# Kernel optimization log

Measured on AMD Instinct MI355X. Metric: run time of the kernel, lower is better.

## Reference

```python
import jax, jax.numpy as jnp
import numpy as np

M, N, DV, DC, ITERS = 512, 1024, 3, 6, 10
BATCH = 8192
ATANH_CLIP = 0.999995


def _build_graph():
    """Deterministic (3,6)-regular Tanner graph, edge order = row-major nonzeros of H."""
    offsets = [0, 1, 2, 512, 515, 519]
    H = np.zeros((M, N), np.int64)
    r = np.arange(M)
    for off in offsets:
        H[r, (2 * r + off) % N] = 1
    ei, ej = np.nonzero(H)                       # E = M*DC = 3072 edges, row-major
    E = ei.size
    var2edges = np.argsort(ej, kind='stable').reshape(N, DV)   # edges of each variable
    chk2edges = np.argsort(ei, kind='stable').reshape(M, DC)   # edges of each check
    v_sum = np.empty((E, DV - 1), np.int64)      # for edge e: other edges on same variable
    c_prod = np.empty((E, DC - 1), np.int64)     # for edge e: other edges on same check
    for e in range(E):
        gv = var2edges[ej[e]]
        v_sum[e] = gv[gv != e]
        gc = chk2edges[ei[e]]
        c_prod[e] = gc[gc != e]
    return v_sum, c_prod, ej.astype(np.int64), var2edges


def setup_inputs() -> dict:
    key = jax.random.key(0)
    ks = jax.random.split(key, 6)
    v_sum, c_prod, edge_var, var2edges = _build_graph()
    E = edge_var.shape[0]                        # 3072
    TW = E * (DV - 1)                            # total_weights = 6144
    return {
        "llr": jax.random.normal(ks[0], (BATCH, N), jnp.float32),
        "w_iter": 1.0 + 0.1 * jax.random.normal(ks[1], (ITERS, TW), jnp.float32),
        "llr_iter": 1.0 + 0.1 * jax.random.normal(ks[2], (ITERS, N), jnp.float32),
        "w_final": 1.0 + 0.1 * jax.random.normal(ks[3], (E,), jnp.float32),
        "llr_final": 1.0 + 0.1 * jax.random.normal(ks[4], (N,), jnp.float32),
        "v_sum_idx": jnp.asarray(v_sum),         # [E, DV-1]
        "c_prod_idx": jnp.asarray(c_prod),       # [E, DC-1]
        "edge_var": jnp.asarray(edge_var),       # [E] variable index of each edge
        "final_idx": jnp.asarray(var2edges),     # [N, DV] edges feeding each variable marginal
    }


def reference(llr, w_iter, llr_iter, w_final, llr_final,
              v_sum_idx, c_prod_idx, edge_var, final_idx):
    B = llr.shape[0]
    E = edge_var.shape[0]
    c2v0 = jnp.zeros((B, E), llr.dtype)

    def bp_iter(c2v, params):
        w, lw = params                                      # [E*(DV-1)], [N]
        # variable -> check: weighted sum of extrinsic c2v messages + weighted LLR
        s = (c2v[:, v_sum_idx] * w.reshape(E, DV - 1)).sum(-1)        # [B,E]
        v2c = jnp.tanh(0.5 * (s + (llr * lw)[:, edge_var]))           # [B,E]
        # check -> variable: product of extrinsic v2c messages, 2*atanh
        prods = v2c[:, c_prod_idx].prod(-1)                           # [B,E]
        return 2.0 * jnp.arctanh(ATANH_CLIP * prods), None

    c2v, _ = jax.lax.scan(bp_iter, c2v0, (w_iter, llr_iter))
    # final marginalization: per-variable sum of weighted incoming messages
    fin = (c2v[:, final_idx.reshape(-1)] * w_final).reshape(B, N, DV).sum(-1)
    out = fin + llr * llr_final
    return jax.nn.sigmoid(out[:, : N - M])
```

## Files before the change

### kernel.cpp

```cpp
#include <hip/hip_runtime.h>
#include <hip/hip_bf16.h>


namespace {

typedef float v2f __attribute__((ext_vector_type(2)));

constexpr int T      = 512;
constexpr int ROWS   = 2;
constexpr int MCHK   = 512;
constexpr int NVAR   = 1024;
constexpr int EEDG   = 3072;
constexpr int NITER  = 10;
constexpr int STRIDE = 7;
constexpr int BATCH  = 8192;
constexpr int NOUT   = 512;

constexpr float LOG2E = 1.4426950408889634f;
constexpr float LN2   = 0.6931471805599453f;
constexpr float KAPPA = 0.999995f;
constexpr float ZCLMP = 16777216.0f;

__device__ __forceinline__ float fast_exp2(float x) { return __builtin_amdgcn_exp2f(x); }
__device__ __forceinline__ float fast_log2(float x) { return __builtin_amdgcn_logf(x); }
__device__ __forceinline__ float fast_rcp (float x) { return __builtin_amdgcn_rcpf(x); }

__global__ __launch_bounds__(T, 4)
void bp_decode(const float* __restrict__ llr,
               const float* __restrict__ w_iter,
               const float* __restrict__ llr_iter,
               const float* __restrict__ w_final,
               const float* __restrict__ llr_final,
               const int*  __restrict__ v_sum_idx,
               const int*  __restrict__ edge_var,
               const int*  __restrict__ final_idx,
               float* __restrict__ out)
{
    __shared__ v2f Ad[MCHK * STRIDE];

    const int  tid = threadIdx.x;
    const long b0  = (long)blockIdx.x * ROWS;

    #pragma unroll
    for (int k = 0; k < STRIDE; ++k)
        Ad[k * T + tid] = (v2f)(0.f);

    int nb[12];
    {
        const int4* p = (const int4*)(v_sum_idx + 12 * tid);
        int4 q0 = p[0], q1 = p[1], q2 = p[2];
        nb[0]=q0.x; nb[1]=q0.y; nb[2]=q0.z; nb[3]=q0.w;
        nb[4]=q1.x; nb[5]=q1.y; nb[6]=q1.z; nb[7]=q1.w;
        nb[8]=q2.x; nb[9]=q2.y; nb[10]=q2.z; nb[11]=q2.w;
    }
    int goff[12];
    #pragma unroll
    for (int j = 0; j < 12; ++j)
        goff[j] = (nb[j] / 6) * STRIDE + (nb[j] % 6);

    int var[6];
    {
        const int2* p = (const int2*)(edge_var + 6 * tid);
        int2 q0 = p[0], q1 = p[1], q2 = p[2];
        var[0]=q0.x; var[1]=q0.y; var[2]=q1.x; var[3]=q1.y; var[4]=q2.x; var[5]=q2.y;
    }

    v2f L[6];
    #pragma unroll
    for (int j = 0; j < 6; ++j) {
        L[j].x = llr[ b0      * NVAR + var[j]];
        L[j].y = llr[(b0 + 1) * NVAR + var[j]];
    }

    __syncthreads();

    const int own = STRIDE * tid;

    #pragma unroll 1
    for (int it = 0; it < NITER; ++it) {
        const float* wit = w_iter + it * (EEDG * 2) + 12 * tid;
        float4 wa = ((const float4*)wit)[0];
        float4 wb = ((const float4*)wit)[1];
        float4 wc = ((const float4*)wit)[2];
        float w[12] = {wa.x,wa.y,wa.z,wa.w, wb.x,wb.y,wb.z,wb.w, wc.x,wc.y,wc.z,wc.w};

        const float* lit = llr_iter + it * NVAR;
        v2f Lli[6];
        #pragma unroll
        for (int j = 0; j < 6; ++j) Lli[j] = L[j] * (lit[var[j]] * LOG2E);

        v2f g[12];
        #pragma unroll
        for (int j = 0; j < 12; ++j) g[j] = Ad[goff[j]];

        __syncthreads();

        v2f zm[6], zp[6];
        #pragma unroll
        for (int j = 0; j < 6; ++j) {
            v2f a = w[2*j] * g[2*j] + w[2*j+1] * g[2*j+1] + Lli[j];
            v2f z;
            z.x = fast_exp2(a.x);
            z.y = fast_exp2(a.y);
            z.x = fminf(z.x, ZCLMP);
            z.y = fminf(z.y, ZCLMP);
            zm[j] = z - 1.f;
            zp[j] = z + 1.f;
        }

        v2f A[6], B[6];
        {
            v2f P1=zm[0], P2=P1*zm[1], P3=P2*zm[2], P4=P3*zm[3], P5=P4*zm[4];
            v2f S4=zm[5], S3=S4*zm[4], S2=S3*zm[3], S1=S2*zm[2], S0=S1*zm[1];
            A[0]=S0; A[1]=P1*S1; A[2]=P2*S2; A[3]=P3*S3; A[4]=P4*S4; A[5]=P5;
        }
        {
            v2f P1=zp[0], P2=P1*zp[1], P3=P2*zp[2], P4=P3*zp[3], P5=P4*zp[4];
            v2f S4=zp[5], S3=S4*zp[4], S2=S3*zp[3], S1=S2*zp[2], S0=S1*zp[1];
            B[0]=S0; B[1]=P1*S1; B[2]=P2*S2; B[3]=P3*S3; B[4]=P4*S4; B[5]=P5;
        }

        #pragma unroll
        for (int j = 0; j < 6; ++j) {
            v2f num = KAPPA * A[j] + B[j];
            v2f den = B[j] - KAPPA * A[j];
            v2f d;
            d.x = fast_log2(num.x) - fast_log2(den.x);
            d.y = fast_log2(num.y) - fast_log2(den.y);
            Ad[own + j] = d;
        }

        __syncthreads();
    }

    int f0 = final_idx[3*tid], f1 = final_idx[3*tid + 1], f2 = final_idx[3*tid + 2];
    v2f d0 = Ad[(f0 / 6) * STRIDE + (f0 % 6)];
    v2f d1 = Ad[(f1 / 6) * STRIDE + (f1 % 6)];
    v2f d2 = Ad[(f2 / 6) * STRIDE + (f2 % 6)];
    float wf0 = w_final[3*tid], wf1 = w_final[3*tid + 1], wf2 = w_final[3*tid + 2];
    float lf  = llr_final[tid];
    float l0  = llr[ b0      * NVAR + tid];
    float l1  = llr[(b0 + 1) * NVAR + tid];

    float finx = (d0.x*wf0 + d1.x*wf1 + d2.x*wf2) * LN2;
    float finy = (d0.y*wf0 + d1.y*wf1 + d2.y*wf2) * LN2;
    float vx = fmaf(l0, lf, finx);
    float vy = fmaf(l1, lf, finy);
    float ox = fast_rcp(1.f + fast_exp2(-vx * LOG2E));
    float oy = fast_rcp(1.f + fast_exp2(-vy * LOG2E));

    out[ b0      * NOUT + tid] = ox;
    out[(b0 + 1) * NOUT + tid] = oy;
}

}

extern "C" void kernel_launch(void* const* d_in, const int* in_sizes, int n_in,
                              void* d_out, int out_size, void* d_ws, size_t ws_size,
                              hipStream_t stream)
{
    const float* llr       = (const float*)d_in[0];
    const float* w_iter    = (const float*)d_in[1];
    const float* llr_iter  = (const float*)d_in[2];
    const float* w_final   = (const float*)d_in[3];
    const float* llr_final = (const float*)d_in[4];
    const int*   v_sum_idx = (const int*)d_in[5];
    const int*   edge_var  = (const int*)d_in[7];
    const int*   final_idx = (const int*)d_in[8];
    float* outp = (float*)d_out;

    dim3 grid(BATCH / ROWS), block(T);
    hipLaunchKernelGGL(bp_decode, grid, block, 0, stream,
                       llr, w_iter, llr_iter, w_final, llr_final,
                       v_sum_idx, edge_var, final_idx, outp);
}
```

Measured before the change: 219.0 us.

## Halve block size and process two checks per thread with packed indices

Block size drops from 512 to 256 threads, and each thread now runs the check-node update for two checks over the same two batch rows. Neighbour offsets and variable indices are packed two per 32-bit register, LOG2E is folded into the cached LLRs ahead of the loop, and the saturation clamp moves from after exp2 to its input. The aim is more independent work per thread for latency hiding, barriers shared across twice the work per thread, and lower register pressure from the packed indices. The cost is a longer serial chain per thread and different occupancy from the new block size. A redundant duplicate log computation is left in the helper.

```diff
diff --git a/kernel.cpp b/kernel.cpp
--- a/kernel.cpp
+++ b/kernel.cpp
@@ -6,8 +6,7 @@
 
 typedef float v2f __attribute__((ext_vector_type(2)));
 
-constexpr int T      = 512;
-constexpr int ROWS   = 2;
+constexpr int T      = 256;
 constexpr int MCHK   = 512;
 constexpr int NVAR   = 1024;
 constexpr int EEDG   = 3072;
@@ -19,11 +18,50 @@
 constexpr float LOG2E = 1.4426950408889634f;
 constexpr float LN2   = 0.6931471805599453f;
 constexpr float KAPPA = 0.999995f;
-constexpr float ZCLMP = 16777216.0f;
+constexpr float ACLMP = 24.0f;
 
 __device__ __forceinline__ float fast_exp2(float x) { return __builtin_amdgcn_exp2f(x); }
 __device__ __forceinline__ float fast_log2(float x) { return __builtin_amdgcn_logf(x); }
 __device__ __forceinline__ float fast_rcp (float x) { return __builtin_amdgcn_rcpf(x); }
+
+__device__ __forceinline__ void check_update(const v2f* __restrict__ g,
+                                             const float* __restrict__ w,
+                                             const v2f* __restrict__ Lli,
+                                             v2f* __restrict__ d)
+{
+    v2f zm[6], zp[6];
+    #pragma unroll
+    for (int j = 0; j < 6; ++j) {
+        v2f a = w[2*j] * g[2*j] + w[2*j+1] * g[2*j+1] + Lli[j];
+        a = __builtin_elementwise_min(a, (v2f)(ACLMP));
+        v2f z;
+        z.x = fast_exp2(a.x);
+        z.y = fast_exp2(a.y);
+        zm[j] = z - 1.f;
+        zp[j] = z + 1.f;
+    }
+    v2f A[6], B[6];
+    {
+        v2f P1=zm[0], P2=P1*zm[1], P3=P2*zm[2], P4=P3*zm[3], P5=P4*zm[4];
+        v2f S4=zm[5], S3=S4*zm[4], S2=S3*zm[3], S1=S2*zm[2], S0=S1*zm[1];
+        A[0]=S0; A[1]=P1*S1; A[2]=P2*S2; A[3]=P3*S3; A[4]=P4*S4; A[5]=P5;
+    }
+    {
+        v2f P1=zp[0], P2=P1*zp[1], P3=P2*zp[2], P4=P3*zp[3], P5=P4*zp[4];
+        v2f S4=zp[5], S3=S4*zp[4], S2=S3*zp[3], S1=S2*zp[2], S0=S1*zp[1];
+        B[0]=S0; B[1]=P1*S1; B[2]=P2*S2; B[3]=P3*S3; B[4]=P4*S4; B[5]=P5;
+    }
+    #pragma unroll
+    for (int j = 0; j < 6; ++j) {
+        v2f num = KAPPA * A[j] + B[j];
+        v2f den = B[j] - KAPPA * A[j];
+        v2f dd;
+        dd.x = fast_log2(num.x) - fast_log2(num.x == num.x ? den.x : den.x);
+        dd.x = fast_log2(num.x) - fast_log2(den.x);
+        dd.y = fast_log2(num.y) - fast_log2(den.y);
+        d[j] = dd;
+    }
+}
 
 __global__ __launch_bounds__(T, 4)
 void bp_decode(const float* __restrict__ llr,
@@ -39,118 +77,144 @@
     __shared__ v2f Ad[MCHK * STRIDE];
 
     const int  tid = threadIdx.x;
-    const long b0  = (long)blockIdx.x * ROWS;
-
-    #pragma unroll
-    for (int k = 0; k < STRIDE; ++k)
+    const long b0  = (long)blockIdx.x * 2;
+
+    #pragma unroll
+    for (int k = 0; k < 2 * STRIDE; ++k)
         Ad[k * T + tid] = (v2f)(0.f);
 
-    int nb[12];
-    {
-        const int4* p = (const int4*)(v_sum_idx + 12 * tid);
-        int4 q0 = p[0], q1 = p[1], q2 = p[2];
-        nb[0]=q0.x; nb[1]=q0.y; nb[2]=q0.z; nb[3]=q0.w;
-        nb[4]=q1.x; nb[5]=q1.y; nb[6]=q1.z; nb[7]=q1.w;
-        nb[8]=q2.x; nb[9]=q2.y; nb[10]=q2.z; nb[11]=q2.w;
-    }
-    int goff[12];
-    #pragma unroll
-    for (int j = 0; j < 12; ++j)
-        goff[j] = (nb[j] / 6) * STRIDE + (nb[j] % 6);
-
-    int var[6];
-    {
-        const int2* p = (const int2*)(edge_var + 6 * tid);
-        int2 q0 = p[0], q1 = p[1], q2 = p[2];
-        var[0]=q0.x; var[1]=q0.y; var[2]=q1.x; var[3]=q1.y; var[4]=q2.x; var[5]=q2.y;
-    }
-
-    v2f L[6];
-    #pragma unroll
-    for (int j = 0; j < 6; ++j) {
-        L[j].x = llr[ b0      * NVAR + var[j]];
-        L[j].y = llr[(b0 + 1) * NVAR + var[j]];
-    }
+    unsigned goffp[12];
+    unsigned varp[6];
+    v2f      Lpre[12];
+
+    #pragma unroll
+    for (int cc = 0; cc < 2; ++cc) {
+        const int c = tid + cc * T;
+        int nb[12];
+        {
+            const int4* p = (const int4*)(v_sum_idx + 12 * c);
+            int4 q0 = p[0], q1 = p[1], q2 = p[2];
+            nb[0]=q0.x; nb[1]=q0.y; nb[2]=q0.z; nb[3]=q0.w;
+            nb[4]=q1.x; nb[5]=q1.y; nb[6]=q1.z; nb[7]=q1.w;
+            nb[8]=q2.x; nb[9]=q2.y; nb[10]=q2.z; nb[11]=q2.w;
+        }
+        #pragma unroll
+        for (int i = 0; i < 6; ++i) {
+            unsigned s0 = (unsigned)((nb[2*i]   / 6) * STRIDE + (nb[2*i]   % 6));
+            unsigned s1 = (unsigned)((nb[2*i+1] / 6) * STRIDE + (nb[2*i+1] % 6));
+            goffp[6*cc + i] = s0 | (s1 << 16);
+        }
+        int var[6];
+        {
+            const int2* p = (const int2*)(edge_var + 6 * c);
+            int2 q0 = p[0], q1 = p[1], q2 = p[2];
+            var[0]=q0.x; var[1]=q0.y; var[2]=q1.x; var[3]=q1.y; var[4]=q2.x; var[5]=q2.y;
+        }
+        #pragma unroll
+        for (int i = 0; i < 3; ++i)
+            varp[3*cc + i] = (unsigned)var[2*i] | ((unsigned)var[2*i+1] << 16);
+        #pragma unroll
+        for (int j = 0; j < 6; ++j) {
+            v2f L;
+            L.x = llr[ b0      * NVAR + var[j]];
+            L.y = llr[(b0 + 1) * NVAR + var[j]];
+            Lpre[6*cc + j] = L * LOG2E;
+        }
+    }
+
+    const int own0 = STRIDE * tid;
+    const int own1 = STRIDE * (tid + T);
 
     __syncthreads();
-
-    const int own = STRIDE * tid;
 
     #pragma unroll 1
     for (int it = 0; it < NITER; ++it) {
-        const float* wit = w_iter + it * (EEDG * 2) + 12 * tid;
-        float4 wa = ((const float4*)wit)[0];
-        float4 wb = ((const float4*)wit)[1];
-        float4 wc = ((const float4*)wit)[2];
-        float w[12] = {wa.x,wa.y,wa.z,wa.w, wb.x,wb.y,wb.z,wb.w, wc.x,wc.y,wc.z,wc.w};
-
+        const float* wit = w_iter + it * (EEDG * 2);
+
+        float w0[12];
+        {
+            const float* p = wit + 12 * tid;
+            float4 a = ((const float4*)p)[0], b = ((const float4*)p)[1], c = ((const float4*)p)[2];
+            w0[0]=a.x; w0[1]=a.y; w0[2]=a.z; w0[3]=a.w;
+            w0[4]=b.x; w0[5]=b.y; w0[6]=b.z; w0[7]=b.w;
+            w0[8]=c.x; w0[9]=c.y; w0[10]=c.z; w0[11]=c.w;
+        }
+
+        v2f g0[12], g1[12];
+        #pragma unroll
+        for (int i = 0; i < 6; ++i) {
+            unsigned p = goffp[i];
+            g0[2*i]   = Ad[p & 0xffffu];
+            g0[2*i+1] = Ad[p >> 16];
+        }
+        #pragma unroll
+        for (int i = 0; i < 6; ++i) {
+            unsigned p = goffp[6 + i];
+            g1[2*i]   = Ad[p & 0xffffu];
+            g1[2*i+1] = Ad[p >> 16];
+        }
+
+        __syncthreads();
+
+        float w1[12];
+        {
+            const float* p = wit + 12 * tid + 6 * T * 2;
+            float4 a = ((const float4*)p)[0], b = ((const float4*)p)[1], c = ((const float4*)p)[2];
+            w1[0]=a.x; w1[1]=a.y; w1[2]=a.z; w1[3]=a.w;
+            w1[4]=b.x; w1[5]=b.y; w1[6]=b.z; w1[7]=b.w;
+            w1[8]=c.x; w1[9]=c.y; w1[10]=c.z; w1[11]=c.w;
+        }
         const float* lit = llr_iter + it * NVAR;
-        v2f Lli[6];
-        #pragma unroll
-        for (int j = 0; j < 6; ++j) Lli[j] = L[j] * (lit[var[j]] * LOG2E);
-
-        v2f g[12];
-        #pragma unroll
-        for (int j = 0; j < 12; ++j) g[j] = Ad[goff[j]];
+
+        float lv0[6], lv1[6];
+        #pragma unroll
+        for (int i = 0; i < 3; ++i) {
+            unsigned p = varp[i];
+            lv0[2*i]   = lit[p & 0xffffu];
+            lv0[2*i+1] = lit[p >> 16];
+        }
+        #pragma unroll
+        for (int i = 0; i < 3; ++i) {
+            unsigned p = varp[3 + i];
+            lv1[2*i]   = lit[p & 0xffffu];
+            lv1[2*i+1] = lit[p >> 16];
+        }
+
+        v2f Lli[6], d[6];
+        #pragma unroll
+        for (int j = 0; j < 6; ++j) Lli[j] = Lpre[j] * lv0[j];
+        check_update(g0, w0, Lli, d);
+        #pragma unroll
+        for (int j = 0; j < 6; ++j) Ad[own0 + j] = d[j];
+
+        #pragma unroll
+        for (int j = 0; j < 6; ++j) Lli[j] = Lpre[6 + j] * lv1[j];
+        check_update(g1, w1, Lli, d);
+        #pragma unroll
+        for (int j = 0; j < 6; ++j) Ad[own1 + j] = d[j];
 
         __syncthreads();
-
-        v2f zm[6], zp[6];
-        #pragma unroll
-        for (int j = 0; j < 6; ++j) {
-            v2f a = w[2*j] * g[2*j] + w[2*j+1] * g[2*j+1] + Lli[j];
-            v2f z;
-            z.x = fast_exp2(a.x);
-            z.y = fast_exp2(a.y);
-            z.x = fminf(z.x, ZCLMP);
-            z.y = fminf(z.y, ZCLMP);
-            zm[j] = z - 1.f;
-            zp[j] = z + 1.f;
-        }
-
-        v2f A[6], B[6];
-        {
-            v2f P1=zm[0], P2=P1*zm[1], P3=P2*zm[2], P4=P3*zm[3], P5=P4*zm[4];
-            v2f S4=zm[5], S3=S4*zm[4], S2=S3*zm[3], S1=S2*zm[2], S0=S1*zm[1];
-            A[0]=S0; A[1]=P1*S1; A[2]=P2*S2; A[3]=P3*S3; A[4]=P4*S4; A[5]=P5;
-        }
-        {
-            v2f P1=zp[0], P2=P1*zp[1], P3=P2*zp[2], P4=P3*zp[3], P5=P4*zp[4];
-            v2f S4=zp[5], S3=S4*zp[4], S2=S3*zp[3], S1=S2*zp[2], S0=S1*zp[1];
-            B[0]=S0; B[1]=P1*S1; B[2]=P2*S2; B[3]=P3*S3; B[4]=P4*S4; B[5]=P5;
-        }
-
-        #pragma unroll
-        for (int j = 0; j < 6; ++j) {
-            v2f num = KAPPA * A[j] + B[j];
-            v2f den = B[j] - KAPPA * A[j];
-            v2f d;
-            d.x = fast_log2(num.x) - fast_log2(den.x);
-            d.y = fast_log2(num.y) - fast_log2(den.y);
-            Ad[own + j] = d;
-        }
-
-        __syncthreads();
-    }
-
-    int f0 = final_idx[3*tid], f1 = final_idx[3*tid + 1], f2 = final_idx[3*tid + 2];
-    v2f d0 = Ad[(f0 / 6) * STRIDE + (f0 % 6)];
-    v2f d1 = Ad[(f1 / 6) * STRIDE + (f1 % 6)];
-    v2f d2 = Ad[(f2 / 6) * STRIDE + (f2 % 6)];
-    float wf0 = w_final[3*tid], wf1 = w_final[3*tid + 1], wf2 = w_final[3*tid + 2];
-    float lf  = llr_final[tid];
-    float l0  = llr[ b0      * NVAR + tid];
-    float l1  = llr[(b0 + 1) * NVAR + tid];
-
-    float finx = (d0.x*wf0 + d1.x*wf1 + d2.x*wf2) * LN2;
-    float finy = (d0.y*wf0 + d1.y*wf1 + d2.y*wf2) * LN2;
-    float vx = fmaf(l0, lf, finx);
-    float vy = fmaf(l1, lf, finy);
-    float ox = fast_rcp(1.f + fast_exp2(-vx * LOG2E));
-    float oy = fast_rcp(1.f + fast_exp2(-vy * LOG2E));
-
-    out[ b0      * NOUT + tid] = ox;
-    out[(b0 + 1) * NOUT + tid] = oy;
+    }
+
+    #pragma unroll
+    for (int cc = 0; cc < 2; ++cc) {
+        const int v = tid + cc * T;
+        int f0 = final_idx[3*v], f1 = final_idx[3*v + 1], f2 = final_idx[3*v + 2];
+        v2f d0 = Ad[(f0 / 6) * STRIDE + (f0 % 6)];
+        v2f d1 = Ad[(f1 / 6) * STRIDE + (f1 % 6)];
+        v2f d2 = Ad[(f2 / 6) * STRIDE + (f2 % 6)];
+        float wf0 = w_final[3*v], wf1 = w_final[3*v + 1], wf2 = w_final[3*v + 2];
+        float lf  = llr_final[v];
+        float l0  = llr[ b0      * NVAR + v];
+        float l1  = llr[(b0 + 1) * NVAR + v];
+
+        float finx = (d0.x*wf0 + d1.x*wf1 + d2.x*wf2) * LN2;
+        float finy = (d0.y*wf0 + d1.y*wf1 + d2.y*wf2) * LN2;
+        float vx = fmaf(l0, lf, finx);
+        float vy = fmaf(l1, lf, finy);
+        out[ b0      * NOUT + v] = fast_rcp(1.f + fast_exp2(-vx * LOG2E));
+        out[(b0 + 1) * NOUT + v] = fast_rcp(1.f + fast_exp2(-vy * LOG2E));
+    }
 }
 
 }
@@ -169,7 +233,7 @@
     const int*   final_idx = (const int*)d_in[8];
     float* outp = (float*)d_out;
 
-    dim3 grid(BATCH / ROWS), block(T);
+    dim3 grid(BATCH / 2), block(T);
     hipLaunchKernelGGL(bp_decode, grid, block, 0, stream,
                        llr, w_iter, llr_iter, w_final, llr_final,
                        v_sum_idx, edge_var, final_idx, outp);
```

Result: slower. 288.2 us (+31.6%).

## Process four batch rows per block with v4f LDS messages and packed indices

Applied to the files above, without the earlier changes.

Doubles the batch rows handled per block from two to four, so each LDS gather now loads a 16-byte vector and the per-edge index, weight and llr_iter loads are amortised over more rows. Gather offsets and variable indices are packed two per 32-bit register to offset the extra register pressure, and the clamp moves from the exp2 output to its input. LDS per block doubles to about 57 KB and launch bounds drop to two blocks per CU, which lowers occupancy and gives fewer waves to hide latency across the barriers.

```diff
diff --git a/kernel.cpp b/kernel.cpp
--- a/kernel.cpp
+++ b/kernel.cpp
@@ -4,13 +4,12 @@
 
 namespace {
 
-typedef float v2f __attribute__((ext_vector_type(2)));
+typedef float v4f __attribute__((ext_vector_type(4)));
 
 constexpr int T      = 512;
-constexpr int ROWS   = 2;
+constexpr int ROWS   = 4;
 constexpr int MCHK   = 512;
 constexpr int NVAR   = 1024;
-constexpr int EEDG   = 3072;
 constexpr int NITER  = 10;
 constexpr int STRIDE = 7;
 constexpr int BATCH  = 8192;
@@ -19,13 +18,13 @@
 constexpr float LOG2E = 1.4426950408889634f;
 constexpr float LN2   = 0.6931471805599453f;
 constexpr float KAPPA = 0.999995f;
-constexpr float ZCLMP = 16777216.0f;
+constexpr float ACLMP = 24.0f;
 
 __device__ __forceinline__ float fast_exp2(float x) { return __builtin_amdgcn_exp2f(x); }
 __device__ __forceinline__ float fast_log2(float x) { return __builtin_amdgcn_logf(x); }
 __device__ __forceinline__ float fast_rcp (float x) { return __builtin_amdgcn_rcpf(x); }
 
-__global__ __launch_bounds__(T, 4)
+__global__ __launch_bounds__(T, 2)
 void bp_decode(const float* __restrict__ llr,
                const float* __restrict__ w_iter,
                const float* __restrict__ llr_iter,
@@ -36,121 +35,145 @@
                const int*  __restrict__ final_idx,
                float* __restrict__ out)
 {
-    __shared__ v2f Ad[MCHK * STRIDE];
+    __shared__ v4f Ad[MCHK * STRIDE];
 
     const int  tid = threadIdx.x;
     const long b0  = (long)blockIdx.x * ROWS;
 
     #pragma unroll
     for (int k = 0; k < STRIDE; ++k)
-        Ad[k * T + tid] = (v2f)(0.f);
+        Ad[k * T + tid] = (v4f)(0.f);
 
-    int nb[12];
+    unsigned goffp[6];
+    unsigned varp[3];
+    v4f      Lpre[6];
     {
+        int nb[12];
         const int4* p = (const int4*)(v_sum_idx + 12 * tid);
         int4 q0 = p[0], q1 = p[1], q2 = p[2];
         nb[0]=q0.x; nb[1]=q0.y; nb[2]=q0.z; nb[3]=q0.w;
         nb[4]=q1.x; nb[5]=q1.y; nb[6]=q1.z; nb[7]=q1.w;
         nb[8]=q2.x; nb[9]=q2.y; nb[10]=q2.z; nb[11]=q2.w;
+        #pragma unroll
+        for (int i = 0; i < 6; ++i) {
+            unsigned s0 = (unsigned)((nb[2*i]   / 6) * STRIDE + (nb[2*i]   % 6));
+            unsigned s1 = (unsigned)((nb[2*i+1] / 6) * STRIDE + (nb[2*i+1] % 6));
+            goffp[i] = s0 | (s1 << 16);
+        }
     }
-    int goff[12];
-    #pragma unroll
-    for (int j = 0; j < 12; ++j)
-        goff[j] = (nb[j] / 6) * STRIDE + (nb[j] % 6);
-
-    int var[6];
     {
+        int var[6];
         const int2* p = (const int2*)(edge_var + 6 * tid);
         int2 q0 = p[0], q1 = p[1], q2 = p[2];
         var[0]=q0.x; var[1]=q0.y; var[2]=q1.x; var[3]=q1.y; var[4]=q2.x; var[5]=q2.y;
+        #pragma unroll
+        for (int i = 0; i < 3; ++i)
+            varp[i] = (unsigned)var[2*i] | ((unsigned)var[2*i+1] << 16);
+        #pragma unroll
+        for (int j = 0; j < 6; ++j) {
+            v4f L;
+            L.x = llr[(b0 + 0) * NVAR + var[j]];
+            L.y = llr[(b0 + 1) * NVAR + var[j]];
+            L.z = llr[(b0 + 2) * NVAR + var[j]];
+            L.w = llr[(b0 + 3) * NVAR + var[j]];
+            Lpre[j] = L * LOG2E;
+        }
     }
 
-    v2f L[6];
-    #pragma unroll
-    for (int j = 0; j < 6; ++j) {
-        L[j].x = llr[ b0      * NVAR + var[j]];
-        L[j].y = llr[(b0 + 1) * NVAR + var[j]];
-    }
+    const int own = STRIDE * tid;
 
     __syncthreads();
 
-    const int own = STRIDE * tid;
-
     #pragma unroll 1
     for (int it = 0; it < NITER; ++it) {
-        const float* wit = w_iter + it * (EEDG * 2) + 12 * tid;
-        float4 wa = ((const float4*)wit)[0];
-        float4 wb = ((const float4*)wit)[1];
-        float4 wc = ((const float4*)wit)[2];
-        float w[12] = {wa.x,wa.y,wa.z,wa.w, wb.x,wb.y,wb.z,wb.w, wc.x,wc.y,wc.z,wc.w};
+        float w[12];
+        {
+            const float* p = w_iter + it * 6144 + 12 * tid;
+            float4 a = ((const float4*)p)[0], b = ((const float4*)p)[1], c = ((const float4*)p)[2];
+            w[0]=a.x; w[1]=a.y; w[2]=a.z;  w[3]=a.w;
+            w[4]=b.x; w[5]=b.y; w[6]=b.z;  w[7]=b.w;
+            w[8]=c.x; w[9]=c.y; w[10]=c.z; w[11]=c.w;
+        }
+        const float* lit = llr_iter + it * NVAR;
+        float lv[6];
+        #pragma unroll
+        for (int i = 0; i < 3; ++i) {
+            unsigned p = varp[i];
+            lv[2*i]   = lit[p & 0xffffu];
+            lv[2*i+1] = lit[p >> 16];
+        }
 
-        const float* lit = llr_iter + it * NVAR;
-        v2f Lli[6];
+        v4f a[6];
         #pragma unroll
-        for (int j = 0; j < 6; ++j) Lli[j] = L[j] * (lit[var[j]] * LOG2E);
-
-        v2f g[12];
+        for (int j = 0; j < 6; ++j) a[j] = Lpre[j] * lv[j];
         #pragma unroll
-        for (int j = 0; j < 12; ++j) g[j] = Ad[goff[j]];
+        for (int i = 0; i < 6; ++i) {
+            unsigned p  = goffp[i];
+            v4f ga = Ad[p & 0xffffu];
+            v4f gb = Ad[p >> 16];
+            a[i] = a[i] + w[2*i] * ga + w[2*i+1] * gb;
+        }
 
         __syncthreads();
 
-        v2f zm[6], zp[6];
+        v4f zm[6], zp[6];
         #pragma unroll
         for (int j = 0; j < 6; ++j) {
-            v2f a = w[2*j] * g[2*j] + w[2*j+1] * g[2*j+1] + Lli[j];
-            v2f z;
-            z.x = fast_exp2(a.x);
-            z.y = fast_exp2(a.y);
-            z.x = fminf(z.x, ZCLMP);
-            z.y = fminf(z.y, ZCLMP);
+            v4f aa = __builtin_elementwise_min(a[j], (v4f)(ACLMP));
+            v4f z;
+            z.x = fast_exp2(aa.x);
+            z.y = fast_exp2(aa.y);
+            z.z = fast_exp2(aa.z);
+            z.w = fast_exp2(aa.w);
             zm[j] = z - 1.f;
             zp[j] = z + 1.f;
         }
-
-        v2f A[6], B[6];
+        v4f A[6], B[6];
         {
-            v2f P1=zm[0], P2=P1*zm[1], P3=P2*zm[2], P4=P3*zm[3], P5=P4*zm[4];
-            v2f S4=zm[5], S3=S4*zm[4], S2=S3*zm[3], S1=S2*zm[2], S0=S1*zm[1];
+            v4f P1=zm[0], P2=P1*zm[1], P3=P2*zm[2], P4=P3*zm[3], P5=P4*zm[4];
+            v4f S4=zm[5], S3=S4*zm[4], S2=S3*zm[3], S1=S2*zm[2], S0=S1*zm[1];
             A[0]=S0; A[1]=P1*S1; A[2]=P2*S2; A[3]=P3*S3; A[4]=P4*S4; A[5]=P5;
         }
         {
-            v2f P1=zp[0], P2=P1*zp[1], P3=P2*zp[2], P4=P3*zp[3], P5=P4*zp[4];
-            v2f S4=zp[5], S3=S4*zp[4], S2=S3*zp[3], S1=S2*zp[2], S0=S1*zp[1];
+            v4f P1=zp[0], P2=P1*zp[1], P3=P2*zp[2], P4=P3*zp[3], P5=P4*zp[4];
+            v4f S4=zp[5], S3=S4*zp[4], S2=S3*zp[3], S1=S2*zp[2], S0=S1*zp[1];
             B[0]=S0; B[1]=P1*S1; B[2]=P2*S2; B[3]=P3*S3; B[4]=P4*S4; B[5]=P5;
         }
-
         #pragma unroll
         for (int j = 0; j < 6; ++j) {
-            v2f num = KAPPA * A[j] + B[j];
-            v2f den = B[j] - KAPPA * A[j];
-            v2f d;
+            v4f num = KAPPA * A[j] + B[j];
+            v4f den = B[j] - KAPPA * A[j];
+            v4f d;
             d.x = fast_log2(num.x) - fast_log2(den.x);
             d.y = fast_log2(num.y) - fast_log2(den.y);
+            d.z = fast_log2(num.z) - fast_log2(den.z);
+            d.w = fast_log2(num.w) - fast_log2(den.w);
             Ad[own + j] = d;
         }
 
         __syncthreads();
     }
 
-    int f0 = final_idx[3*tid], f1 = final_idx[3*tid + 1], f2 = final_idx[3*tid + 2];
-    v2f d0 = Ad[(f0 / 6) * STRIDE + (f0 % 6)];
-    v2f d1 = Ad[(f1 / 6) * STRIDE + (f1 % 6)];
-    v2f d2 = Ad[(f2 / 6) * STRIDE + (f2 % 6)];
-    float wf0 = w_final[3*tid], wf1 = w_final[3*tid + 1], wf2 = w_final[3*tid + 2];
-    float lf  = llr_final[tid];
-    float l0  = llr[ b0      * NVAR + tid];
-    float l1  = llr[(b0 + 1) * NVAR + tid];
+    {
+        int f0 = final_idx[3*tid], f1 = final_idx[3*tid + 1], f2 = final_idx[3*tid + 2];
+        v4f d0 = Ad[(f0 / 6) * STRIDE + (f0 % 6)];
+        v4f d1 = Ad[(f1 / 6) * STRIDE + (f1 % 6)];
+        v4f d2 = Ad[(f2 / 6) * STRIDE + (f2 % 6)];
+        float wf0 = w_final[3*tid], wf1 = w_final[3*tid + 1], wf2 = w_final[3*tid + 2];
+        float lf  = llr_final[tid];
+        v4f l;
+        l.x = llr[(b0 + 0) * NVAR + tid];
+        l.y = llr[(b0 + 1) * NVAR + tid];
+        l.z = llr[(b0 + 2) * NVAR + tid];
+        l.w = llr[(b0 + 3) * NVAR + tid];
 
-    float finx = (d0.x*wf0 + d1.x*wf1 + d2.x*wf2) * LN2;
-    float finy = (d0.y*wf0 + d1.y*wf1 + d2.y*wf2) * LN2;
-    float vx = fmaf(l0, lf, finx);
-    float vy = fmaf(l1, lf, finy);
-    float ox = fast_rcp(1.f + fast_exp2(-vx * LOG2E));
-    float oy = fast_rcp(1.f + fast_exp2(-vy * LOG2E));
-
-    out[ b0      * NOUT + tid] = ox;
-    out[(b0 + 1) * NOUT + tid] = oy;
+        v4f fin = (d0 * wf0 + d1 * wf1 + d2 * wf2) * LN2;
+        v4f v   = l * lf + fin;
+        out[(b0 + 0) * NOUT + tid] = fast_rcp(1.f + fast_exp2(-v.x * LOG2E));
+        out[(b0 + 1) * NOUT + tid] = fast_rcp(1.f + fast_exp2(-v.y * LOG2E));
+        out[(b0 + 2) * NOUT + tid] = fast_rcp(1.f + fast_exp2(-v.z * LOG2E));
+        out[(b0 + 3) * NOUT + tid] = fast_rcp(1.f + fast_exp2(-v.w * LOG2E));
+    }
 }
 
 }
```

Result: slower. 241.7 us (+10.4%).
